# Optimization experiments

Measured on AMD Instinct MI355X. Metric: run time of the kernel, lower is better.

Reference implementation:

```python
import jax, jax.numpy as jnp
import numpy as np

B, N, NODE_DIM, COND_DIM, EDGE_DIM = 16, 256, 512, 512, 128
E_TOT = 262144  # total edges, divisible by B
EPS = 1e-5


def weight_norm(v, g):
    # torch weight_norm dim=0: per-output-row normalization. v: [out, in], g: [out]
    return v * (g / jnp.sqrt(jnp.sum(v * v, axis=1)))[:, None]


def setup_inputs() -> dict:
    key = jax.random.key(0)
    ks = jax.random.split(key, 12)
    node_feats = jax.random.normal(ks[0], (B, N, NODE_DIM), dtype=jnp.float32)
    cond_feats = jax.random.normal(ks[1], (B, COND_DIM), dtype=jnp.float32)
    edge_indexes = jnp.sort(jax.random.randint(ks[2], (E_TOT,), 0, B * N * N, dtype=jnp.int64))
    s_node = 1.0 / np.sqrt(NODE_DIM)
    s_cond = 1.0 / np.sqrt(COND_DIM)
    s_film = 1.0 / np.sqrt(2 * EDGE_DIM)
    return {
        "node_feats": node_feats,
        "cond_feats": cond_feats,
        "edge_indexes": edge_indexes,
        "v_node": jax.random.uniform(ks[3], (EDGE_DIM, NODE_DIM), jnp.float32, -s_node, s_node),
        "g_node": jnp.ones((EDGE_DIM,), jnp.float32),
        "b_node": jnp.zeros((EDGE_DIM,), jnp.float32),
        "v_cond": jax.random.uniform(ks[4], (2 * EDGE_DIM, COND_DIM), jnp.float32, -s_cond, s_cond),
        "g_cond": jnp.ones((2 * EDGE_DIM,), jnp.float32),
        "b_cond": jnp.zeros((2 * EDGE_DIM,), jnp.float32),
        "w_film": jax.random.uniform(ks[5], (EDGE_DIM, 2 * EDGE_DIM), jnp.float32, -s_film, s_film),
        "b_film": jnp.zeros((EDGE_DIM,), jnp.float32),
    }


def reference(node_feats, cond_feats, edge_indexes, v_node, g_node, b_node,
              v_cond, g_cond, b_cond, w_film, b_film):
    # node projection: Dropout(0) -> weight_norm Linear -> ReLU
    w_n = weight_norm(v_node, g_node)
    nodes = jax.nn.relu(jnp.einsum('bnd,ed->bne', node_feats, w_n) + b_node)  # [B,N,E]

    # cond projection -> gamma, beta
    w_c = weight_norm(v_cond, g_cond)
    gb = cond_feats @ w_c.T + b_cond  # [B, 2E]
    gamma = gb[:, :EDGE_DIM] + 1.0
    beta = gb[:, EDGE_DIM:]

    # gather edge endpoints directly (equivalent to materializing [B,N,N,2E] 'cat' then indexing)
    b_idx = edge_indexes // (N * N)
    i_idx = (edge_indexes // N) % N
    j_idx = edge_indexes % N
    fused = jnp.concatenate([nodes[b_idx, i_idx], nodes[b_idx, j_idx]], axis=-1)  # [E_TOT, 2E]

    # film_l: linear -> LayerNorm(no affine) -> FiLM -> ReLU, on view (B, E_TOT//B, E)
    x = fused @ w_film.T + b_film  # [E_TOT, EDGE_DIM]
    x = x.reshape(B, E_TOT // B, EDGE_DIM)
    mu = jnp.mean(x, axis=-1, keepdims=True)
    var = jnp.mean(jnp.square(x - mu), axis=-1, keepdims=True)
    x = (x - mu) * jax.lax.rsqrt(var + EPS)
    x = x * gamma[:, None, :] + beta[:, None, :]
    x = jax.nn.relu(x)
    return x.reshape(E_TOT, EDGE_DIM)
```

## Files before the change

### kernel.cpp

```cpp
#include <hip/hip_runtime.h>
#include <hip/hip_bf16.h>

typedef __bf16 bf16_t;
typedef bf16_t bf16x8 __attribute__((ext_vector_type(8)));
typedef bf16_t bf16x4 __attribute__((ext_vector_type(4)));
typedef float f32x4 __attribute__((ext_vector_type(4)));

#define NODE_DIM 512
#define COND_DIM 512
#define EDGE_DIM 128

#define WS_A    0x000000
#define WS_WN   0x400000
#define WS_WC   0x420000
#define WS_SC   0x430000
#define WS_GA   0x431000
#define WS_BE   0x433000
#define WS_P    0x440000

__device__ __forceinline__ bf16x8 cvt8(float4 a, float4 b) {
    bf16x8 v;
    v[0] = (bf16_t)a.x; v[1] = (bf16_t)a.y; v[2] = (bf16_t)a.z; v[3] = (bf16_t)a.w;
    v[4] = (bf16_t)b.x; v[5] = (bf16_t)b.y; v[6] = (bf16_t)b.z; v[7] = (bf16_t)b.w;
    return v;
}

__global__ __launch_bounds__(256) void prep_kernel(
    const float* __restrict__ node_feats, const float* __restrict__ cond_feats,
    const float* __restrict__ v_node, const float* __restrict__ g_node,
    const float* __restrict__ v_cond, const float* __restrict__ g_cond,
    const float* __restrict__ b_cond, const float* __restrict__ w_film,
    char* __restrict__ ws)
{
    bf16_t* A  = (bf16_t*)(ws + WS_A);
    bf16_t* Wn = (bf16_t*)(ws + WS_WN);
    bf16_t* Wc = (bf16_t*)(ws + WS_WC);
    float* scale_node = (float*)(ws + WS_SC);
    float* gamma = (float*)(ws + WS_GA);
    float* beta  = (float*)(ws + WS_BE);

    int t = threadIdx.x;
    int bid = blockIdx.x;
    int lane = t & 63, wv = t >> 6;

    if (bid < 1024) {
        size_t idx = ((size_t)bid * 256 + t) * 8;
        float4 a = ((const float4*)(node_feats + idx))[0];
        float4 b = ((const float4*)(node_feats + idx))[1];
        *(bf16x8*)(A + idx) = cvt8(a, b);
    } else if (bid < 1056) {
        size_t idx = ((size_t)(bid - 1024) * 256 + t) * 8;
        float4 a = ((const float4*)(v_node + idx))[0];
        float4 b = ((const float4*)(v_node + idx))[1];
        *(bf16x8*)(Wn + idx) = cvt8(a, b);
    } else if (bid < 1072) {
        int u = (bid - 1056) * 256 + t;
        int n = u >> 4;
        int ko = (u & 15) * 8;
        const float* src = (n < 128) ? (w_film + (size_t)n * 256 + ko)
                                     : (w_film + (size_t)(n - 128) * 256 + 128 + ko);
        float4 a = ((const float4*)src)[0];
        float4 b = ((const float4*)src)[1];
        *(bf16x8*)(Wc + (size_t)n * 128 + ko) = cvt8(a, b);
    } else if (bid < 1104) {
        int id = (bid - 1072) * 4 + wv;
        const float* vn = v_node + (size_t)id * NODE_DIM + lane * 8;
        float sq = 0.f;
#pragma unroll
        for (int i = 0; i < 2; i++) {
            float4 v4 = ((const float4*)vn)[i];
            sq += v4.x * v4.x + v4.y * v4.y + v4.z * v4.z + v4.w * v4.w;
        }
#pragma unroll
        for (int o = 32; o > 0; o >>= 1) sq += __shfl_xor(sq, o);
        if (lane == 0) scale_node[id] = g_node[id] * rsqrtf(sq);
    } else {
        int id = (bid - 1104) * 4 + wv;
        int b = id >> 8, n = id & 255;
        const float* cf = cond_feats + b * COND_DIM + lane * 8;
        const float* vc = v_cond + (size_t)n * COND_DIM + lane * 8;
        float dot = 0.f, sq = 0.f;
#pragma unroll
        for (int i = 0; i < 2; i++) {
            float4 c4 = ((const float4*)cf)[i];
            float4 v4 = ((const float4*)vc)[i];
            dot += c4.x * v4.x + c4.y * v4.y + c4.z * v4.z + c4.w * v4.w;
            sq  += v4.x * v4.x + v4.y * v4.y + v4.z * v4.z + v4.w * v4.w;
        }
#pragma unroll
        for (int o = 32; o > 0; o >>= 1) {
            dot += __shfl_xor(dot, o);
            sq  += __shfl_xor(sq, o);
        }
        if (lane == 0) {
            float val = dot * (g_cond[n] * rsqrtf(sq)) + b_cond[n];
            if (n < 128) gamma[b * 128 + n] = val + 1.0f;
            else         beta[b * 128 + (n - 128)] = val;
        }
    }
}

__global__ __launch_bounds__(256) void gemm_kernel(
    const float* __restrict__ b_node, char* __restrict__ ws)
{
    const bf16_t* A  = (const bf16_t*)(ws + WS_A);
    const bf16_t* Wn = (const bf16_t*)(ws + WS_WN);
    const bf16_t* Wc = (const bf16_t*)(ws + WS_WC);
    const float* scale_node = (const float*)(ws + WS_SC);
    bf16_t* P = (bf16_t*)(ws + WS_P);

    __shared__ __attribute__((aligned(16))) bf16_t N_s[16 * 136];
    __shared__ __attribute__((aligned(16))) float  T_s[4][16][68];

    int t = threadIdx.x;
    int lane = t & 63, w = t >> 6;
    int r16 = lane & 15, half = lane >> 4;
    int m0 = blockIdx.x * 16;

    f32x4 zero4 = {0.f, 0.f, 0.f, 0.f};

    f32x4 acc0 = zero4, acc1 = zero4;
    {
        const bf16_t* aptr = A + (size_t)(m0 + r16) * NODE_DIM + half * 8;
        const bf16_t* bptr = Wn + (size_t)(w * 32 + r16) * NODE_DIM + half * 8;
#pragma unroll
        for (int ks = 0; ks < 16; ks++) {
            bf16x8 af = *(const bf16x8*)(aptr + ks * 32);
            bf16x8 b0 = *(const bf16x8*)(bptr + ks * 32);
            bf16x8 b1 = *(const bf16x8*)(bptr + 16 * NODE_DIM + ks * 32);
            acc0 = __builtin_amdgcn_mfma_f32_16x16x32_bf16(af, b0, acc0, 0, 0, 0);
            acc1 = __builtin_amdgcn_mfma_f32_16x16x32_bf16(af, b1, acc1, 0, 0, 0);
        }
    }
    {
        int rbase = half * 4;
#pragma unroll
        for (int j = 0; j < 2; j++) {
            int col = w * 32 + j * 16 + r16;
            float s = scale_node[col], bb = b_node[col];
            f32x4 a = j ? acc1 : acc0;
#pragma unroll
            for (int r = 0; r < 4; r++) {
                float v = fmaxf(a[r] * s + bb, 0.f);
                N_s[(rbase + r) * 136 + col] = (bf16_t)v;
            }
        }
    }
    __syncthreads();

    f32x4 acc2[4];
#pragma unroll
    for (int i = 0; i < 4; i++) acc2[i] = zero4;
    {
        const bf16_t* bptr = Wc + (size_t)(w * 64 + r16) * 128 + half * 8;
#pragma unroll
        for (int ks = 0; ks < 4; ks++) {
            bf16x8 af = *(const bf16x8*)&N_s[r16 * 136 + ks * 32 + half * 8];
#pragma unroll
            for (int j = 0; j < 4; j++) {
                bf16x8 bf = *(const bf16x8*)(bptr + j * 16 * 128 + ks * 32);
                acc2[j] = __builtin_amdgcn_mfma_f32_16x16x32_bf16(af, bf, acc2[j], 0, 0, 0);
            }
        }
    }
    {
        int rbase = half * 4;
#pragma unroll
        for (int j = 0; j < 4; j++) {
            int col = j * 16 + r16;
#pragma unroll
            for (int r = 0; r < 4; r++) T_s[w][rbase + r][col] = acc2[j][r];
        }
    }
    __syncthreads();
    {
#pragma unroll
        for (int r2 = 0; r2 < 2; r2++) {
            int row = r2 * 8 + (lane >> 3);
            int colg = (lane & 7) * 8;
            float4 a = *(const float4*)&T_s[w][row][colg];
            float4 b = *(const float4*)&T_s[w][row][colg + 4];
            *(bf16x8*)&P[(size_t)(m0 + row) * 256 + w * 64 + colg] = cvt8(a, b);
        }
    }
}

__global__ __launch_bounds__(256) void edge_kernel(
    const int* __restrict__ edges, const char* __restrict__ ws,
    const float* __restrict__ b_film, float* __restrict__ out)
{
    const bf16_t* P = (const bf16_t*)(ws + WS_P);
    const float* gamma = (const float*)(ws + WS_GA);
    const float* beta  = (const float*)(ws + WS_BE);

    int t = threadIdx.x;
    int lane = t & 63, wv = t >> 6;
    int v = (blockIdx.x & 7) * 4096 + (blockIdx.x >> 3);
    int r = v * 8 + wv * 2 + (lane >> 5);
    int hl = lane & 31;
    int c = hl * 4;

    int bb = v >> 11;
    float4 g4  = *(const float4*)&gamma[bb * 128 + c];
    float4 be4 = *(const float4*)&beta[bb * 128 + c];
    float4 bf4 = *(const float4*)&b_film[c];

    int e = edges[r];
    int ri = e >> 8;
    int rj = ((e >> 16) << 8) | (e & 255);

    bf16x4 p1 = *(const bf16x4*)&P[(size_t)ri * 256 + c];
    bf16x4 p2 = *(const bf16x4*)&P[(size_t)rj * 256 + 128 + c];

    float x0 = (float)p1[0] + (float)p2[0] + bf4.x;
    float x1 = (float)p1[1] + (float)p2[1] + bf4.y;
    float x2 = (float)p1[2] + (float)p2[2] + bf4.z;
    float x3 = (float)p1[3] + (float)p2[3] + bf4.w;

    float s  = x0 + x1 + x2 + x3;
    float ss = x0 * x0 + x1 * x1 + x2 * x2 + x3 * x3;
#pragma unroll
    for (int o = 16; o > 0; o >>= 1) {
        s  += __shfl_xor(s, o);
        ss += __shfl_xor(ss, o);
    }
    float mu  = s * (1.0f / 128.0f);
    float var = ss * (1.0f / 128.0f) - mu * mu;
    float rs  = rsqrtf(var + 1e-5f);

    float4 o4;
    o4.x = fmaxf((x0 - mu) * rs * g4.x + be4.x, 0.f);
    o4.y = fmaxf((x1 - mu) * rs * g4.y + be4.y, 0.f);
    o4.z = fmaxf((x2 - mu) * rs * g4.z + be4.z, 0.f);
    o4.w = fmaxf((x3 - mu) * rs * g4.w + be4.w, 0.f);
    *(float4*)&out[(size_t)r * 128 + c] = o4;
}

extern "C" void kernel_launch(void* const* d_in, const int* in_sizes, int n_in,
                              void* d_out, int out_size, void* d_ws, size_t ws_size,
                              hipStream_t stream) {
    const float* node_feats = (const float*)d_in[0];
    const float* cond_feats = (const float*)d_in[1];
    const int*   edges      = (const int*)d_in[2];
    const float* v_node     = (const float*)d_in[3];
    const float* g_node     = (const float*)d_in[4];
    const float* b_node     = (const float*)d_in[5];
    const float* v_cond     = (const float*)d_in[6];
    const float* g_cond     = (const float*)d_in[7];
    const float* b_cond     = (const float*)d_in[8];
    const float* w_film     = (const float*)d_in[9];
    const float* b_film     = (const float*)d_in[10];
    float* out = (float*)d_out;
    char* ws = (char*)d_ws;

    prep_kernel<<<2128, 256, 0, stream>>>(node_feats, cond_feats, v_node, g_node,
                                          v_cond, g_cond, b_cond, w_film, ws);
    gemm_kernel<<<256, 256, 0, stream>>>(b_node, ws);
    edge_kernel<<<32768, 256, 0, stream>>>(edges, ws, b_film, out);
}
```

Baseline: 195.2 us.

## Fuse node_feats bf16 conversion into GEMM and use nontemporal output stores

```diff
diff --git a/kernel.cpp b/kernel.cpp
--- a/kernel.cpp
+++ b/kernel.cpp
@@ -10,13 +10,12 @@
 #define COND_DIM 512
 #define EDGE_DIM 128
 
-#define WS_A    0x000000
-#define WS_WN   0x400000
-#define WS_WC   0x420000
-#define WS_SC   0x430000
-#define WS_GA   0x431000
-#define WS_BE   0x433000
-#define WS_P    0x440000
+#define WS_WN   0x000000
+#define WS_WC   0x020000
+#define WS_SC   0x030000
+#define WS_GA   0x031000
+#define WS_BE   0x033000
+#define WS_P    0x040000
 
 __device__ __forceinline__ bf16x8 cvt8(float4 a, float4 b) {
     bf16x8 v;
@@ -26,13 +25,12 @@
 }
 
 __global__ __launch_bounds__(256) void prep_kernel(
-    const float* __restrict__ node_feats, const float* __restrict__ cond_feats,
+    const float* __restrict__ cond_feats,
     const float* __restrict__ v_node, const float* __restrict__ g_node,
     const float* __restrict__ v_cond, const float* __restrict__ g_cond,
     const float* __restrict__ b_cond, const float* __restrict__ w_film,
     char* __restrict__ ws)
 {
-    bf16_t* A  = (bf16_t*)(ws + WS_A);
     bf16_t* Wn = (bf16_t*)(ws + WS_WN);
     bf16_t* Wc = (bf16_t*)(ws + WS_WC);
     float* scale_node = (float*)(ws + WS_SC);
@@ -43,18 +41,13 @@
     int bid = blockIdx.x;
     int lane = t & 63, wv = t >> 6;
 
-    if (bid < 1024) {
+    if (bid < 32) {
         size_t idx = ((size_t)bid * 256 + t) * 8;
-        float4 a = ((const float4*)(node_feats + idx))[0];
-        float4 b = ((const float4*)(node_feats + idx))[1];
-        *(bf16x8*)(A + idx) = cvt8(a, b);
-    } else if (bid < 1056) {
-        size_t idx = ((size_t)(bid - 1024) * 256 + t) * 8;
         float4 a = ((const float4*)(v_node + idx))[0];
         float4 b = ((const float4*)(v_node + idx))[1];
         *(bf16x8*)(Wn + idx) = cvt8(a, b);
-    } else if (bid < 1072) {
-        int u = (bid - 1056) * 256 + t;
+    } else if (bid < 48) {
+        int u = (bid - 32) * 256 + t;
         int n = u >> 4;
         int ko = (u & 15) * 8;
         const float* src = (n < 128) ? (w_film + (size_t)n * 256 + ko)
@@ -62,8 +55,8 @@
         float4 a = ((const float4*)src)[0];
         float4 b = ((const float4*)src)[1];
         *(bf16x8*)(Wc + (size_t)n * 128 + ko) = cvt8(a, b);
-    } else if (bid < 1104) {
-        int id = (bid - 1072) * 4 + wv;
+    } else if (bid < 80) {
+        int id = (bid - 48) * 4 + wv;
         const float* vn = v_node + (size_t)id * NODE_DIM + lane * 8;
         float sq = 0.f;
 #pragma unroll
@@ -75,7 +68,7 @@
         for (int o = 32; o > 0; o >>= 1) sq += __shfl_xor(sq, o);
         if (lane == 0) scale_node[id] = g_node[id] * rsqrtf(sq);
     } else {
-        int id = (bid - 1104) * 4 + wv;
+        int id = (bid - 80) * 4 + wv;
         int b = id >> 8, n = id & 255;
         const float* cf = cond_feats + b * COND_DIM + lane * 8;
         const float* vc = v_cond + (size_t)n * COND_DIM + lane * 8;
@@ -101,9 +94,9 @@
 }
 
 __global__ __launch_bounds__(256) void gemm_kernel(
-    const float* __restrict__ b_node, char* __restrict__ ws)
+    const float* __restrict__ node_feats, const float* __restrict__ b_node,
+    char* __restrict__ ws)
 {
-    const bf16_t* A  = (const bf16_t*)(ws + WS_A);
     const bf16_t* Wn = (const bf16_t*)(ws + WS_WN);
     const bf16_t* Wc = (const bf16_t*)(ws + WS_WC);
     const float* scale_node = (const float*)(ws + WS_SC);
@@ -121,11 +114,13 @@
 
     f32x4 acc0 = zero4, acc1 = zero4;
     {
-        const bf16_t* aptr = A + (size_t)(m0 + r16) * NODE_DIM + half * 8;
+        const float*  aptr = node_feats + (size_t)(m0 + r16) * NODE_DIM + half * 8;
         const bf16_t* bptr = Wn + (size_t)(w * 32 + r16) * NODE_DIM + half * 8;
 #pragma unroll
         for (int ks = 0; ks < 16; ks++) {
-            bf16x8 af = *(const bf16x8*)(aptr + ks * 32);
+            float4 a0 = ((const float4*)(aptr + ks * 32))[0];
+            float4 a1 = ((const float4*)(aptr + ks * 32))[1];
+            bf16x8 af = cvt8(a0, a1);
             bf16x8 b0 = *(const bf16x8*)(bptr + ks * 32);
             bf16x8 b1 = *(const bf16x8*)(bptr + 16 * NODE_DIM + ks * 32);
             acc0 = __builtin_amdgcn_mfma_f32_16x16x32_bf16(af, b0, acc0, 0, 0, 0);
@@ -228,12 +223,12 @@
     float var = ss * (1.0f / 128.0f) - mu * mu;
     float rs  = rsqrtf(var + 1e-5f);
 
-    float4 o4;
-    o4.x = fmaxf((x0 - mu) * rs * g4.x + be4.x, 0.f);
-    o4.y = fmaxf((x1 - mu) * rs * g4.y + be4.y, 0.f);
-    o4.z = fmaxf((x2 - mu) * rs * g4.z + be4.z, 0.f);
-    o4.w = fmaxf((x3 - mu) * rs * g4.w + be4.w, 0.f);
-    *(float4*)&out[(size_t)r * 128 + c] = o4;
+    f32x4 o4;
+    o4[0] = fmaxf((x0 - mu) * rs * g4.x + be4.x, 0.f);
+    o4[1] = fmaxf((x1 - mu) * rs * g4.y + be4.y, 0.f);
+    o4[2] = fmaxf((x2 - mu) * rs * g4.z + be4.z, 0.f);
+    o4[3] = fmaxf((x3 - mu) * rs * g4.w + be4.w, 0.f);
+    __builtin_nontemporal_store(o4, (f32x4*)&out[(size_t)r * 128 + c]);
 }
 
 extern "C" void kernel_launch(void* const* d_in, const int* in_sizes, int n_in,
@@ -253,8 +248,8 @@
     float* out = (float*)d_out;
     char* ws = (char*)d_ws;
 
-    prep_kernel<<<2128, 256, 0, stream>>>(node_feats, cond_feats, v_node, g_node,
+    prep_kernel<<<1104, 256, 0, stream>>>(cond_feats, v_node, g_node,
                                           v_cond, g_cond, b_cond, w_film, ws);
-    gemm_kernel<<<256, 256, 0, stream>>>(b_node, ws);
+    gemm_kernel<<<256, 256, 0, stream>>>(node_feats, b_node, ws);
     edge_kernel<<<32768, 256, 0, stream>>>(edges, ws, b_film, out);
 }
```

New measurement: 201.8 us. 1.03x slower.
